# Performance work log

Hardware: AMD Instinct MI355X
Metric: run time of the kernel (lower is better)

The kernel has to match this reference:

```python
import jax, jax.numpy as jnp
import numpy as np

H = 128; D = 16; L = 4
NP_ = 50000; NL_ = 10000; EPP = 500000; ELP = 100000; EPL = 100000


def _rbf(d):
    # GaussianSmearing(start=0, stop=8, num_gaussians=16)
    off = jnp.linspace(0.0, 8.0, D)
    coeff = -0.5 / ((8.0 / (D - 1)) ** 2)
    x = d[:, None] - off[None, :]
    return jnp.exp(coeff * x * x)


def _layer_norm(x, w, b, eps=1e-5):
    mu = jnp.mean(x, axis=-1, keepdims=True)
    var = jnp.var(x, axis=-1, keepdims=True)
    return (x - mu) * jax.lax.rsqrt(var + eps) * w + b


def _block(x_src, x_dst, src, dst, ea, Wf_, bf_, Ws_, bs_, bnw, bnb, lnw, lnb):
    # CGConv message: z = [x_i(dst), x_j(src), edge_attr]
    z = jnp.concatenate([x_dst[dst], x_src[src], ea], axis=-1)  # [E, 2H+D]
    m = jax.nn.sigmoid(z @ Wf_ + bf_) * jax.nn.softplus(z @ Ws_ + bs_)
    agg = jax.ops.segment_sum(m, dst, num_segments=x_dst.shape[0])
    # BatchNorm1d in eval mode with running_mean=0, running_var=1
    agg = agg * (bnw / jnp.sqrt(1.0 + 1e-5)) + bnb
    out = agg + x_dst            # CGConv internal residual
    out = _layer_norm(out, lnw, lnb)
    out = jax.nn.relu(out)
    return out + x_dst           # ResidualCGConvBlock residual (dropout=identity in eval)


def setup_inputs() -> dict:
    key = jax.random.key(0)
    ks = jax.random.split(key, 16)
    s = lambda n: 1.0 / np.sqrt(n)
    inp = {
        'x_protein': jax.random.normal(ks[0], (NP_, 6), jnp.float32),
        'x_ligand': jax.random.normal(ks[1], (NL_, 6), jnp.float32),
        'ei_pp': jnp.stack([jax.random.randint(ks[2], (EPP,), 0, NP_),
                            jax.random.randint(ks[3], (EPP,), 0, NP_)]).astype(jnp.int32),
        'ea_pp': jax.random.uniform(ks[4], (EPP,), jnp.float32, 0.0, 8.0),
        'ei_lp': jnp.stack([jax.random.randint(ks[5], (ELP,), 0, NL_),
                            jax.random.randint(ks[6], (ELP,), 0, NP_)]).astype(jnp.int32),
        'ea_lp': jax.random.uniform(ks[7], (ELP,), jnp.float32, 0.0, 8.0),
        'ei_pl': jnp.stack([jax.random.randint(ks[8], (EPL,), 0, NP_),
                            jax.random.randint(ks[9], (EPL,), 0, NL_)]).astype(jnp.int32),
        'ea_pl': jax.random.uniform(ks[10], (EPL,), jnp.float32, 0.0, 8.0),
        'Wp': jax.random.normal(ks[11], (6, H), jnp.float32) * s(6),
        'bp': jnp.zeros((H,), jnp.float32),
        'Wl': jax.random.normal(ks[12], (6, H), jnp.float32) * s(6),
        'bl': jnp.zeros((H,), jnp.float32),
        'Wf': jax.random.normal(ks[13], (L, 3, 2 * H + D, H), jnp.float32) * s(2 * H + D),
        'bf': jnp.zeros((L, 3, H), jnp.float32),
        'Ws': jax.random.normal(ks[14], (L, 3, 2 * H + D, H), jnp.float32) * s(2 * H + D),
        'bs': jnp.zeros((L, 3, H), jnp.float32),
        'bn_w': jnp.ones((L, 3, H), jnp.float32),
        'bn_b': jnp.zeros((L, 3, H), jnp.float32),
        'ln_w': jnp.ones((L, 3, H), jnp.float32),
        'ln_b': jnp.zeros((L, 3, H), jnp.float32),
        'lno_w': jnp.ones((H,), jnp.float32),
        'lno_b': jnp.zeros((H,), jnp.float32),
        'fc_w': jax.random.normal(ks[15], (H, 21), jnp.float32) * s(H),
        'fc_b': jnp.zeros((21,), jnp.float32),
    }
    return inp


def reference(x_protein, x_ligand, ei_pp, ea_pp, ei_lp, ea_lp, ei_pl, ea_pl,
              Wp, bp, Wl, bl, Wf, bf, Ws, bs, bn_w, bn_b, ln_w, ln_b,
              lno_w, lno_b, fc_w, fc_b):
    xp = x_protein @ Wp + bp
    xl = x_ligand @ Wl + bl
    rpp = _rbf(ea_pp); rlp = _rbf(ea_lp); rpl = _rbf(ea_pl)
    for l in range(L):
        # HeteroConv aggr='sum': protein receives from pp and lp; ligand from pl
        p_pp = _block(xp, xp, ei_pp[0], ei_pp[1], rpp, Wf[l, 0], bf[l, 0], Ws[l, 0], bs[l, 0],
                      bn_w[l, 0], bn_b[l, 0], ln_w[l, 0], ln_b[l, 0])
        p_lp = _block(xl, xp, ei_lp[0], ei_lp[1], rlp, Wf[l, 1], bf[l, 1], Ws[l, 1], bs[l, 1],
                      bn_w[l, 1], bn_b[l, 1], ln_w[l, 1], ln_b[l, 1])
        l_pl = _block(xp, xl, ei_pl[0], ei_pl[1], rpl, Wf[l, 2], bf[l, 2], Ws[l, 2], bs[l, 2],
                      bn_w[l, 2], bn_b[l, 2], ln_w[l, 2], ln_b[l, 2])
        xp, xl = p_pp + p_lp, l_pl
    out = _layer_norm(xp, lno_w, lno_b)
    return out @ fc_w + fc_b
```

## Files before the change

### kernel.cpp

```cpp
#include <hip/hip_runtime.h>
#include <hip/hip_bf16.h>
#include <math.h>

#define H 128
#define LOG2E 1.44269504f

typedef __bf16 bf16x8 __attribute__((ext_vector_type(8)));
typedef float f32x4 __attribute__((ext_vector_type(4)));
typedef float f32x2 __attribute__((ext_vector_type(2)));
typedef __hip_bfloat16 bf16;
typedef unsigned int uint32;

static __device__ __forceinline__ float bf2f(bf16 v){ return __bfloat162float(v); }
static __device__ __forceinline__ bf16 f2bf(float v){ return __float2bfloat16(v); }
static __device__ __forceinline__ float u2f_lo(uint32 v){ return __uint_as_float(v << 16); }
static __device__ __forceinline__ float u2f_hi(uint32 v){ return __uint_as_float(v & 0xffff0000u); }

union bfpack { struct { bf16 lo, hi; } h; uint32 u; };
static __device__ __forceinline__ uint32 pack_bf2(float a, float b){
  bfpack p; p.h.lo = f2bf(a); p.h.hi = f2bf(b); return p.u;
}

static __device__ __forceinline__ int unperm64(int r){
  int base = r & ~63; int g = r & 63; int t = g >> 4; int j = g & 15;
  return base + 4*j + t;
}

#define NBIN 256
#define PREP_WP_N (4*1024*128)
#define PREP_WL_N (4*512*128)
#define RBF_N     (12*(NBIN+1)*128)

__global__ void prep_all(const float* __restrict__ Wf, const float* __restrict__ Ws,
                         const float* __restrict__ bfv, const float* __restrict__ bsv,
                         bf16* __restrict__ Wt_p, float* __restrict__ Bias_p,
                         bf16* __restrict__ Wt_l, float* __restrict__ Bias_l,
                         bf16* __restrict__ T2,
                         const float* __restrict__ Xp, const float* __restrict__ Wp,
                         const float* __restrict__ bp, float* __restrict__ Xpo,
                         bf16* __restrict__ Xpb, int NP,
                         const float* __restrict__ Xl, const float* __restrict__ Wl,
                         const float* __restrict__ bl, float* __restrict__ Xlo,
                         bf16* __restrict__ Xlb, int NL){
  int t = blockIdx.x*blockDim.x + threadIdx.x;
  if (t < PREP_WP_N){
    int k = t & 127; int idx = t >> 7;
    int rs = idx & 1023; int l = idx >> 10;
    int r = unperm64(rs);
    int rel, c, row0; const float* W; float bias = 0.f;
    if (r < 256)      { rel=0; c=r>>1;        row0=128; W = (r&1)?Ws:Wf; }
    else if (r < 512) { rel=2; c=(r-256)>>1;  row0=128; W = (r&1)?Ws:Wf; }
    else if (r < 640) { rel=0; c=r-512; row0=0; W=Wf; bias = bfv[(l*3+rel)*H+c]; }
    else if (r < 768) { rel=0; c=r-640; row0=0; W=Ws; bias = bsv[(l*3+rel)*H+c]; }
    else if (r < 896) { rel=1; c=r-768; row0=0; W=Wf; bias = bfv[(l*3+rel)*H+c]; }
    else              { rel=1; c=r-896; row0=0; W=Ws; bias = bsv[(l*3+rel)*H+c]; }
    Wt_p[t] = f2bf(LOG2E * W[((size_t)(l*3+rel)*272 + row0 + k)*H + c]);
    if (k == 0) Bias_p[l*1024 + r] = LOG2E * bias;
    return;
  }
  t -= PREP_WP_N;
  if (t < PREP_WL_N){
    int k = t & 127; int idx = t >> 7;
    int rs = idx & 511; int l = idx >> 9;
    int r = unperm64(rs);
    int rel, c, row0; const float* W; float bias = 0.f;
    if (r < 256)      { rel=1; c=r>>1;   row0=128; W = (r&1)?Ws:Wf; }
    else if (r < 384) { rel=2; c=r-256; row0=0; W=Wf; bias = bfv[(l*3+rel)*H+c]; }
    else              { rel=2; c=r-384; row0=0; W=Ws; bias = bsv[(l*3+rel)*H+c]; }
    Wt_l[t] = f2bf(LOG2E * W[((size_t)(l*3+rel)*272 + row0 + k)*H + c]);
    if (k == 0) Bias_l[l*512 + r] = LOG2E * bias;
    return;
  }
  t -= PREP_WL_N;
  if (t < RBF_N){
    int c = t & 127;
    int b = (t >> 7) % (NBIN+1);
    int pr = t / ((NBIN+1)*128);
    float d0 = (float)b * (8.0f/(float)NBIN);
    const float* wf = Wf + ((size_t)pr*272 + 256)*H + c;
    const float* ws = Ws + ((size_t)pr*272 + 256)*H + c;
    float f0=0.f, s0=0.f;
    #pragma unroll
    for (int k=0;k<16;k++){
      float o = 0.533333333f*(float)k;
      float tt = d0 - o;
      float r0 = __expf(-1.7578125f*tt*tt);
      f0 += r0*wf[(size_t)k*H]; s0 += r0*ws[(size_t)k*H];
    }
    bf16* o = T2 + ((size_t)(pr*(NBIN+1) + b))*256 + 2*c;
    o[0]=f2bf(LOG2E * f0); o[1]=f2bf(LOG2E * s0);
    return;
  }
  t -= RBF_N;
  {
    int idx = t;
    const float* Xin; const float* W; const float* b; float* Xout; bf16* Xbf;
    if (idx < NP*H){ Xin=Xp; W=Wp; b=bp; Xout=Xpo; Xbf=Xpb; }
    else { idx -= NP*H; if (idx >= NL*H) return; Xin=Xl; W=Wl; b=bl; Xout=Xlo; Xbf=Xlb; }
    int n = idx >> 7, c = idx & 127;
    float acc = b[c];
    #pragma unroll
    for (int k=0;k<6;k++) acc += Xin[n*6+k] * W[k*H+c];
    Xout[idx] = acc;
    Xbf[idx] = f2bf(acc);
  }
}

__global__ void hist3_k(const int* __restrict__ dpp, int Epp,
                        const int* __restrict__ dlp, int Elp,
                        const int* __restrict__ dpl, int Epl,
                        int* __restrict__ cpp, int* __restrict__ clp, int* __restrict__ cpl){
  int e = blockIdx.x*blockDim.x + threadIdx.x;
  if (e < Epp) atomicAdd(&cpp[dpp[e]], 1);
  else if (e < Epp+Elp) atomicAdd(&clp[dlp[e-Epp]], 1);
  else if (e < Epp+Elp+Epl) atomicAdd(&cpl[dpl[e-Epp-Elp]], 1);
}

#define SCH 1024

__global__ void __launch_bounds__(256) chunksum_k(
    const int* __restrict__ counts, int NP, int NL, int Cpp, int Cpl,
    int* __restrict__ chsum){
  __shared__ int wred[4];
  int b = blockIdx.x;
  const int* cnt; int n; int ch;
  if (b < Cpp){ cnt = counts; n = NP; ch = b; }
  else if (b < 2*Cpp){ cnt = counts + NP; n = NP; ch = b - Cpp; }
  else { cnt = counts + 2*NP; n = NL; ch = b - 2*Cpp; }
  int base = ch * SCH;
  int tid = threadIdx.x;
  int s = 0;
  #pragma unroll
  for (int j=0;j<SCH/256;j++){
    int i = base + tid + j*256;
    if (i < n) s += cnt[i];
  }
  #pragma unroll
  for (int o=32;o>=1;o>>=1) s += __shfl_xor(s,o,64);
  if ((tid & 63) == 0) wred[tid>>6] = s;
  __syncthreads();
  if (tid == 0) chsum[b] = wred[0]+wred[1]+wred[2]+wred[3];
}

__global__ void __launch_bounds__(192) scanmid_k(
    int* __restrict__ chsum, int Cpp, int Cpl, int NP, int NL,
    int* __restrict__ rp_pp, int* __restrict__ rp_lp, int* __restrict__ rp_pl){
  int wid = threadIdx.x >> 6, lane = threadIdx.x & 63;
  int C, off; int* rp_end; int n;
  if (wid == 0){ C = Cpp; off = 0;      rp_end = rp_pp; n = NP; }
  else if (wid == 1){ C = Cpp; off = Cpp; rp_end = rp_lp; n = NP; }
  else { C = Cpl; off = 2*Cpp; rp_end = rp_pl; n = NL; }
  int v = (lane < C) ? chsum[off + lane] : 0;
  int x = v;
  #pragma unroll
  for (int o=1;o<64;o<<=1){
    int y = __shfl_up(x, o, 64);
    if (lane >= o) x += y;
  }
  if (lane < C) chsum[off + lane] = x - v;
  if (lane == 63) rp_end[n] = x;
}

__global__ void __launch_bounds__(1024) scanfin_k(
    const int* __restrict__ counts, int NP, int NL, int Cpp, int Cpl,
    const int* __restrict__ chsum,
    int* __restrict__ rp_pp, int* __restrict__ cur_pp,
    int* __restrict__ rp_lp, int* __restrict__ cur_lp,
    int* __restrict__ rp_pl, int* __restrict__ cur_pl){
  __shared__ int wsum[16];
  int b = blockIdx.x;
  const int* cnt; int n, ch; int* rp; int* cur;
  if (b < Cpp){ cnt = counts; n = NP; ch = b; rp = rp_pp; cur = cur_pp; }
  else if (b < 2*Cpp){ cnt = counts + NP; n = NP; ch = b - Cpp; rp = rp_lp; cur = cur_lp; }
  else { cnt = counts + 2*NP; n = NL; ch = b - 2*Cpp; rp = rp_pl; cur = cur_pl; }
  int tid = threadIdx.x, lane = tid & 63, wid = tid >> 6;
  int i = ch*SCH + tid;
  int v = (i < n) ? cnt[i] : 0;
  int x = v;
  #pragma unroll
  for (int o=1;o<64;o<<=1){
    int y = __shfl_up(x, o, 64);
    if (lane >= o) x += y;
  }
  if (lane == 63) wsum[wid] = x;
  __syncthreads();
  if (wid == 0 && lane < 16){
    int w = wsum[lane];
    #pragma unroll
    for (int o=1;o<16;o<<=1){
      int y = __shfl_up(w, o, 64);
      if (lane >= o) w += y;
    }
    wsum[lane] = w;
  }
  __syncthreads();
  int waveoff = (wid == 0) ? 0 : wsum[wid-1];
  int ex = chsum[b] + waveoff + x - v;
  if (i < n){ rp[i] = ex; cur[i] = ex; }
}

__global__ void fill3_k(const int* __restrict__ ei_pp, const float* __restrict__ ea_pp, int Epp,
                        const int* __restrict__ ei_lp, const float* __restrict__ ea_lp, int Elp,
                        const int* __restrict__ ei_pl, const float* __restrict__ ea_pl, int Epl,
                        int* __restrict__ cur_pp, int2* __restrict__ e2_pp,
                        int* __restrict__ cur_lp, int2* __restrict__ e2_lp,
                        int* __restrict__ cur_pl, int2* __restrict__ e2_pl){
  int e = blockIdx.x*blockDim.x + threadIdx.x;
  if (e < Epp){
    int p = atomicAdd(&cur_pp[ei_pp[Epp + e]], 1);
    e2_pp[p] = make_int2(ei_pp[e], __float_as_int(ea_pp[e]));
  } else if (e < Epp+Elp){
    int i = e - Epp;
    int p = atomicAdd(&cur_lp[ei_lp[Elp + i]], 1);
    e2_lp[p] = make_int2(ei_lp[i], __float_as_int(ea_lp[i]));
  } else if (e < Epp+Elp+Epl){
    int i = e - Epp - Elp;
    int p = atomicAdd(&cur_pl[ei_pl[Epl + i]], 1);
    e2_pl[p] = make_int2(ei_pl[i], __float_as_int(ea_pl[i]));
  }
}

#define GR 8
__global__ void __launch_bounds__(256) gemm_tables(
    const bf16* __restrict__ Xp, const bf16* __restrict__ Wtp,
    const float* __restrict__ Biasp, bf16* __restrict__ Outp,
    int strips_p, int tasks_p,
    const bf16* __restrict__ Xl, const bf16* __restrict__ Wtl,
    const float* __restrict__ Biasl, bf16* __restrict__ Outl,
    int strips_l, int tasks_total){
  int wt = blockIdx.x*4 + (threadIdx.x >> 6);
  if (wt >= tasks_total) return;
  const bf16 *X, *Wt; const float* Bias; bf16* Out; int N, strips, g, chunk;
  if (wt < tasks_p){
    X=Xp; Wt=Wtp; Bias=Biasp; Out=Outp; N=1024; strips=strips_p;
    g = wt & 15; chunk = wt >> 4;
  } else {
    int w = wt - tasks_p;
    X=Xl; Wt=Wtl; Bias=Biasl; Out=Outl; N=512; strips=strips_l;
    g = w & 7; chunk = w >> 3;
  }
  int n0 = g << 6;
  int lane = threadIdx.x & 63;
  int lr = lane & 15, lq = lane >> 4;
  const bf16x8* B0 = (const bf16x8*)(const void*)(Wt + (size_t)(n0      + lr)*H);
  const bf16x8* B1 = (const bf16x8*)(const void*)(Wt + (size_t)(n0 + 16 + lr)*H);
  const bf16x8* B2 = (const bf16x8*)(const void*)(Wt + (size_t)(n0 + 32 + lr)*H);
  const bf16x8* B3 = (const bf16x8*)(const void*)(Wt + (size_t)(n0 + 48 + lr)*H);
  bf16x8 b0_0=B0[lq], b0_1=B0[4+lq], b0_2=B0[8+lq], b0_3=B0[12+lq];
  bf16x8 b1_0=B1[lq], b1_1=B1[4+lq], b1_2=B1[8+lq], b1_3=B1[12+lq];
  bf16x8 b2_0=B2[lq], b2_1=B2[4+lq], b2_2=B2[8+lq], b2_3=B2[12+lq];
  bf16x8 b3_0=B3[lq], b3_1=B3[4+lq], b3_2=B3[8+lq], b3_3=B3[12+lq];
  float4 bias = ((const float4*)(const void*)(Bias + n0))[lr];
  #pragma unroll 2
  for (int r=0;r<GR;r++){
    int strip = chunk*GR + r;
    if (strip >= strips) break;
    int m0 = strip << 4;
    const bf16x8* A = (const bf16x8*)(const void*)(X + (size_t)(m0+lr)*H);
    bf16x8 a0 = A[lq], a1 = A[4+lq], a2 = A[8+lq], a3 = A[12+lq];
    f32x4 acc0 = {0.f,0.f,0.f,0.f}, acc1 = acc0, acc2 = acc0, acc3 = acc0;
    acc0 = __builtin_amdgcn_mfma_f32_16x16x32_bf16(a0, b0_0, acc0, 0, 0, 0);
    acc1 = __builtin_amdgcn_mfma_f32_16x16x32_bf16(a0, b1_0, acc1, 0, 0, 0);
    acc2 = __builtin_amdgcn_mfma_f32_16x16x32_bf16(a0, b2_0, acc2, 0, 0, 0);
    acc3 = __builtin_amdgcn_mfma_f32_16x16x32_bf16(a0, b3_0, acc3, 0, 0, 0);
    acc0 = __builtin_amdgcn_mfma_f32_16x16x32_bf16(a1, b0_1, acc0, 0, 0, 0);
    acc1 = __builtin_amdgcn_mfma_f32_16x16x32_bf16(a1, b1_1, acc1, 0, 0, 0);
    acc2 = __builtin_amdgcn_mfma_f32_16x16x32_bf16(a1, b2_1, acc2, 0, 0, 0);
    acc3 = __builtin_amdgcn_mfma_f32_16x16x32_bf16(a1, b3_1, acc3, 0, 0, 0);
    acc0 = __builtin_amdgcn_mfma_f32_16x16x32_bf16(a2, b0_2, acc0, 0, 0, 0);
    acc1 = __builtin_amdgcn_mfma_f32_16x16x32_bf16(a2, b1_2, acc1, 0, 0, 0);
    acc2 = __builtin_amdgcn_mfma_f32_16x16x32_bf16(a2, b2_2, acc2, 0, 0, 0);
    acc3 = __builtin_amdgcn_mfma_f32_16x16x32_bf16(a2, b3_2, acc3, 0, 0, 0);
    acc0 = __builtin_amdgcn_mfma_f32_16x16x32_bf16(a3, b0_3, acc0, 0, 0, 0);
    acc1 = __builtin_amdgcn_mfma_f32_16x16x32_bf16(a3, b1_3, acc1, 0, 0, 0);
    acc2 = __builtin_amdgcn_mfma_f32_16x16x32_bf16(a3, b2_3, acc2, 0, 0, 0);
    acc3 = __builtin_amdgcn_mfma_f32_16x16x32_bf16(a3, b3_3, acc3, 0, 0, 0);
    #pragma unroll
    for (int rr=0;rr<4;rr++){
      int row = m0 + lq*4 + rr;
      uint2 pk;
      pk.x = pack_bf2(acc0[rr] + bias.x, acc1[rr] + bias.y);
      pk.y = pack_bf2(acc2[rr] + bias.z, acc3[rr] + bias.w);
      *(uint2*)(void*)(Out + (size_t)row*N + n0 + 4*lr) = pk;
    }
  }
}

static __device__ __forceinline__ float act_msg(float F, float S){
  float sig = __builtin_amdgcn_rcpf(1.f + __builtin_amdgcn_exp2f(-F));
  float e   = __builtin_amdgcn_exp2f(fminf(S, 86.f));
  float sp  = 0.69314718f * __builtin_amdgcn_logf(1.f + e);
  return sig * sp;
}

#define BN_RSQ 0.9999950000374997f

static __device__ __forceinline__ void edge_nb(uint2 g, uint2 t,
                                               f32x2 fd2, f32x2 sd2, f32x2& acc){
  f32x2 f2, s2;
  f2.x = u2f_lo(g.x) + u2f_lo(t.x);
  f2.y = u2f_lo(g.y) + u2f_lo(t.y);
  s2.x = u2f_hi(g.x) + u2f_hi(t.x);
  s2.y = u2f_hi(g.y) + u2f_hi(t.y);
  f2 += fd2; s2 += sd2;
  acc.x += act_msg(f2.x, s2.x);
  acc.y += act_msg(f2.y, s2.y);
}

static __device__ __forceinline__ void ln_stats_w(float v0, float v1, float& mu, float& var){
  float s = v0 + v1, q = v0*v0 + v1*v1;
  #pragma unroll
  for (int o=32;o>=1;o>>=1){ s += __shfl_xor(s,o,64); q += __shfl_xor(q,o,64); }
  mu = s * (1.f/128.f);
  var = q * (1.f/128.f) - mu*mu;
}

static __device__ __forceinline__ void aggregate(
    const int2* __restrict__ ev_arr, int e0, int e1,
    const uint2* __restrict__ G, int gstride, int goff,
    const uint2* __restrict__ Tb, int lane,
    f32x2 fd2, f32x2 sd2, f32x2& acc)
{
  for (int base = e0; base < e1; base += 64){
    int idx = base + lane;
    int2 ev = ev_arr[(idx < e1) ? idx : (e1-1)];
    float dd = __int_as_float(ev.y);
    int bnv = (int)__fmaf_rn(dd, (float)NBIN/8.0f, 0.5f);
    bnv = (bnv > NBIN) ? NBIN : bnv;
    int cnt = e1 - base; cnt = (cnt > 64) ? 64 : cnt;
    uint2 gA, tA, gB, tB, gC, tC;
    #define LDJ(gX, tX, j) { \
      int s_ = __builtin_amdgcn_readlane(ev.x, (j)); \
      int b_ = __builtin_amdgcn_readlane(bnv, (j)); \
      gX = G[(size_t)s_*gstride + goff + lane]; \
      tX = Tb[(size_t)b_*64 + lane]; }
    LDJ(gA, tA, 0);
    if (cnt > 1) LDJ(gB, tB, 1);
    if (cnt > 2) LDJ(gC, tC, 2);
    int j = 0;
    for (; j+5 < cnt; j += 3){
      edge_nb(gA, tA, fd2, sd2, acc); LDJ(gA, tA, j+3);
      edge_nb(gB, tB, fd2, sd2, acc); LDJ(gB, tB, j+4);
      edge_nb(gC, tC, fd2, sd2, acc); LDJ(gC, tC, j+5);
    }
    int rem = cnt - j;
    edge_nb(gA, tA, fd2, sd2, acc);
    if (rem > 3) LDJ(gA, tA, j+3);
    if (rem > 1) edge_nb(gB, tB, fd2, sd2, acc);
    if (rem > 4) LDJ(gB, tB, j+4);
    if (rem > 2) edge_nb(gC, tC, fd2, sd2, acc);
    if (rem > 3) edge_nb(gA, tA, fd2, sd2, acc);
    if (rem > 4) edge_nb(gB, tB, fd2, sd2, acc);
    #undef LDJ
  }
}

__global__ void __launch_bounds__(256) node_update(
    const bf16* __restrict__ PT, const bf16* __restrict__ LT,
    const float* __restrict__ xp, const float* __restrict__ xl,
    const int* __restrict__ pp_rp, const int2* __restrict__ pp_e2,
    const int* __restrict__ lp_rp, const int2* __restrict__ lp_e2,
    const int* __restrict__ pl_rp, const int2* __restrict__ pl_e2,
    const bf16* __restrict__ T2,
    const float* __restrict__ bn_w, const float* __restrict__ bn_b,
    const float* __restrict__ ln_w, const float* __restrict__ ln_b,
    float* __restrict__ xp_out, bf16* __restrict__ xp_bf,
    float* __restrict__ xl_out, bf16* __restrict__ xl_bf,
    int layer, int NP, int NL, int PB)
{
  int wave = threadIdx.x >> 6;
  int lane = threadIdx.x & 63;
  const uint2* PTg = (const uint2*)(const void*)PT;
  if ((int)blockIdx.x < PB){
    int node = blockIdx.x*4 + wave;
    if (node >= NP) return;
    float2 x = ((const float2*)(const void*)(xp + (size_t)node*H))[lane];
    const uint32* PTu = (const uint32*)(const void*)PT;
    const uint2*  LTg = (const uint2*)(const void*)LT;
    float o1_0, o1_1, o2_0, o2_1;
    {
      int pr = layer*3 + 0;
      uint32 fdp = PTu[(size_t)node*512 + 256 + lane];
      uint32 sdp = PTu[(size_t)node*512 + 320 + lane];
      const uint2* Tb = (const uint2*)(const void*)(T2 + (size_t)pr*(NBIN+1)*256);
      f32x2 fd2 = {u2f_lo(fdp), u2f_hi(fdp)};
      f32x2 sd2 = {u2f_lo(sdp), u2f_hi(sdp)};
      f32x2 acc = {0.f, 0.f};
      aggregate(pp_e2, pp_rp[node], pp_rp[node+1], PTg, 256, 0, Tb, lane, fd2, sd2, acc);
      float2 bw = ((const float2*)(const void*)(bn_w + pr*H))[lane];
      float2 bb = ((const float2*)(const void*)(bn_b + pr*H))[lane];
      float2 lw = ((const float2*)(const void*)(ln_w + pr*H))[lane];
      float2 lb = ((const float2*)(const void*)(ln_b + pr*H))[lane];
      float v0 = acc.x * (bw.x * BN_RSQ) + bb.x + x.x;
      float v1 = acc.y * (bw.y * BN_RSQ) + bb.y + x.y;
      float mu, var; ln_stats_w(v0, v1, mu, var);
      float rs = rsqrtf(var + 1e-5f);
      o1_0 = fmaxf((v0-mu)*rs*lw.x + lb.x, 0.f) + x.x;
      o1_1 = fmaxf((v1-mu)*rs*lw.y + lb.y, 0.f) + x.y;
    }
    {
      int pr = layer*3 + 1;
      uint32 fdp = PTu[(size_t)node*512 + 384 + lane];
      uint32 sdp = PTu[(size_t)node*512 + 448 + lane];
      const uint2* Tb = (const uint2*)(const void*)(T2 + (size_t)pr*(NBIN+1)*256);
      f32x2 fd2 = {u2f_lo(fdp), u2f_hi(fdp)};
      f32x2 sd2 = {u2f_lo(sdp), u2f_hi(sdp)};
      f32x2 acc = {0.f, 0.f};
      aggregate(lp_e2, lp_rp[node], lp_rp[node+1], LTg, 128, 0, Tb, lane, fd2, sd2, acc);
      float2 bw = ((const float2*)(const void*)(bn_w + pr*H))[lane];
      float2 bb = ((const float2*)(const void*)(bn_b + pr*H))[lane];
      float2 lw = ((const float2*)(const void*)(ln_w + pr*H))[lane];
      float2 lb = ((const float2*)(const void*)(ln_b + pr*H))[lane];
      float v0 = acc.x * (bw.x * BN_RSQ) + bb.x + x.x;
      float v1 = acc.y * (bw.y * BN_RSQ) + bb.y + x.y;
      float mu, var; ln_stats_w(v0, v1, mu, var);
      float rs = rsqrtf(var + 1e-5f);
      o2_0 = fmaxf((v0-mu)*rs*lw.x + lb.x, 0.f) + x.x;
      o2_1 = fmaxf((v1-mu)*rs*lw.y + lb.y, 0.f) + x.y;
    }
    float out0 = o1_0 + o2_0, out1 = o1_1 + o2_1;
    ((float2*)(void*)(xp_out + (size_t)node*H))[lane] = make_float2(out0, out1);
    ((uint32*)(void*)(xp_bf + (size_t)node*H))[lane] = pack_bf2(out0, out1);
  } else {
    int node = (blockIdx.x - PB)*4 + wave;
    if (node >= NL) return;
    float2 x = ((const float2*)(const void*)(xl + (size_t)node*H))[lane];
    const uint32* LTu = (const uint32*)(const void*)LT;
    int pr = layer*3 + 2;
    uint32 fdp = LTu[(size_t)node*256 + 128 + lane];
    uint32 sdp = LTu[(size_t)node*256 + 192 + lane];
    const uint2* Tb = (const uint2*)(const void*)(T2 + (size_t)pr*(NBIN+1)*256);
    f32x2 fd2 = {u2f_lo(fdp), u2f_hi(fdp)};
    f32x2 sd2 = {u2f_lo(sdp), u2f_hi(sdp)};
    f32x2 acc = {0.f, 0.f};
    aggregate(pl_e2, pl_rp[node], pl_rp[node+1], PTg, 256, 64, Tb, lane, fd2, sd2, acc);
    float2 bw = ((const float2*)(const void*)(bn_w + pr*H))[lane];
    float2 bb = ((const float2*)(const void*)(bn_b + pr*H))[lane];
    float2 lw = ((const float2*)(const void*)(ln_w + pr*H))[lane];
    float2 lb = ((const float2*)(const void*)(ln_b + pr*H))[lane];
    float v0 = acc.x * (bw.x * BN_RSQ) + bb.x + x.x;
    float v1 = acc.y * (bw.y * BN_RSQ) + bb.y + x.y;
    float mu, var; ln_stats_w(v0, v1, mu, var);
    float rs = rsqrtf(var + 1e-5f);
    float out0 = fmaxf((v0-mu)*rs*lw.x + lb.x, 0.f) + x.x;
    float out1 = fmaxf((v1-mu)*rs*lw.y + lb.y, 0.f) + x.y;
    ((float2*)(void*)(xl_out + (size_t)node*H))[lane] = make_float2(out0, out1);
    ((uint32*)(void*)(xl_bf + (size_t)node*H))[lane] = pack_bf2(out0, out1);
  }
}

__global__ void __launch_bounds__(128) final_k(const float* __restrict__ xp,
    const float* __restrict__ lnw, const float* __restrict__ lnb,
    const float* __restrict__ fcw, const float* __restrict__ fcb,
    float* __restrict__ out, int N){
  __shared__ float sm[4];
  __shared__ float lnv[128];
  int node = blockIdx.x, c = threadIdx.x;
  float v = xp[(size_t)node*H + c];
  float s = v, q = v*v;
  #pragma unroll
  for (int o=32;o>=1;o>>=1){ s += __shfl_xor(s,o,64); q += __shfl_xor(q,o,64); }
  __syncthreads();
  if ((c & 63) == 0){ sm[(c>>6)*2] = s; sm[(c>>6)*2+1] = q; }
  __syncthreads();
  float S = sm[0] + sm[2], Q = sm[1] + sm[3];
  float mu = S * (1.f/128.f);
  float var = Q * (1.f/128.f) - mu*mu;
  float ln = (v-mu)*rsqrtf(var+1e-5f)*lnw[c] + lnb[c];
  lnv[c] = ln;
  __syncthreads();
  if (c < 21){
    float a = fcb[c];
    #pragma unroll 4
    for (int i=0;i<128;i++) a += lnv[i]*fcw[i*21+c];
    out[(size_t)node*21 + c] = a;
  }
}

extern "C" void kernel_launch(void* const* d_in, const int* in_sizes, int n_in,
                              void* d_out, int out_size, void* d_ws, size_t ws_size,
                              hipStream_t stream){
  const float* x_protein = (const float*)d_in[0];
  const float* x_ligand  = (const float*)d_in[1];
  const int*   ei_pp = (const int*)d_in[2];
  const float* ea_pp = (const float*)d_in[3];
  const int*   ei_lp = (const int*)d_in[4];
  const float* ea_lp = (const float*)d_in[5];
  const int*   ei_pl = (const int*)d_in[6];
  const float* ea_pl = (const float*)d_in[7];
  const float* Wp  = (const float*)d_in[8];
  const float* bp  = (const float*)d_in[9];
  const float* Wl  = (const float*)d_in[10];
  const float* bl  = (const float*)d_in[11];
  const float* Wf  = (const float*)d_in[12];
  const float* bfv = (const float*)d_in[13];
  const float* Wsv = (const float*)d_in[14];
  const float* bsv = (const float*)d_in[15];
  const float* bn_w = (const float*)d_in[16];
  const float* bn_b = (const float*)d_in[17];
  const float* ln_w = (const float*)d_in[18];
  const float* ln_b = (const float*)d_in[19];
  const float* lno_w = (const float*)d_in[20];
  const float* lno_b = (const float*)d_in[21];
  const float* fc_w = (const float*)d_in[22];
  const float* fc_b = (const float*)d_in[23];

  int NP  = in_sizes[0]/6, NL = in_sizes[1]/6;
  int EPP = in_sizes[3], ELP = in_sizes[5], EPL = in_sizes[7];

  char* ws = (char*)d_ws;
  size_t off = 0;
  auto alloc = [&](size_t bytes)->void*{
    void* p = ws + off; off = (off + bytes + 255) & ~(size_t)255; return p;
  };

  float* xpA = (float*)alloc((size_t)NP*H*4);
  float* xpB = (float*)alloc((size_t)NP*H*4);
  float* xlA = (float*)alloc((size_t)NL*H*4);
  float* xlB = (float*)alloc((size_t)NL*H*4);
  bf16* xp_bf = (bf16*)alloc((size_t)NP*H*2);
  bf16* xl_bf = (bf16*)alloc((size_t)NL*H*2);
  bf16* PT    = (bf16*)alloc((size_t)NP*1024*2);
  bf16* LT    = (bf16*)alloc((size_t)NL*512*2);
  bf16* Wt_p  = (bf16*)alloc((size_t)4*1024*H*2);
  bf16* Wt_l  = (bf16*)alloc((size_t)4*512*H*2);
  float* Bias_p = (float*)alloc((size_t)4*1024*4);
  float* Bias_l = (float*)alloc((size_t)4*512*4);
  bf16* T2    = (bf16*)alloc((size_t)12*(NBIN+1)*256*2);
  int* counts = (int*)alloc((size_t)(2*NP+NL)*4);
  int* rp_pp  = (int*)alloc((size_t)(NP+1)*4);
  int* cur_pp = (int*)alloc((size_t)NP*4);
  int* rp_lp  = (int*)alloc((size_t)(NP+1)*4);
  int* cur_lp = (int*)alloc((size_t)NP*4);
  int* rp_pl  = (int*)alloc((size_t)(NL+1)*4);
  int* cur_pl = (int*)alloc((size_t)NL*4);
  int2* e2_pp = (int2*)alloc((size_t)EPP*8);
  int2* e2_lp = (int2*)alloc((size_t)ELP*8);
  int2* e2_pl = (int2*)alloc((size_t)EPL*8);
  int Cpp = (NP + SCH - 1) / SCH;
  int Cpl = (NL + SCH - 1) / SCH;
  int* chsum = (int*)alloc((size_t)(2*Cpp + Cpl)*4);
  (void)ws_size; (void)n_in; (void)out_size;

  size_t prep_total = (size_t)PREP_WP_N + PREP_WL_N + RBF_N + (size_t)(NP+NL)*H;
  prep_all<<<(prep_total+255)/256, 256, 0, stream>>>(Wf, Wsv, bfv, bsv,
      Wt_p, Bias_p, Wt_l, Bias_l, T2,
      x_protein, Wp, bp, xpA, xp_bf, NP,
      x_ligand,  Wl, bl, xlA, xl_bf, NL);
  hipMemsetAsync(counts, 0, (size_t)(2*NP+NL)*4, stream);
  int* cnt_pp = counts; int* cnt_lp = counts + NP; int* cnt_pl = counts + 2*NP;
  int Etot = EPP + ELP + EPL;
  hist3_k<<<(Etot+255)/256, 256, 0, stream>>>(ei_pp+EPP, EPP, ei_lp+ELP, ELP, ei_pl+EPL, EPL,
                                              cnt_pp, cnt_lp, cnt_pl);
  chunksum_k<<<2*Cpp + Cpl, 256, 0, stream>>>(counts, NP, NL, Cpp, Cpl, chsum);
  scanmid_k<<<1, 192, 0, stream>>>(chsum, Cpp, Cpl, NP, NL, rp_pp, rp_lp, rp_pl);
  scanfin_k<<<2*Cpp + Cpl, 1024, 0, stream>>>(counts, NP, NL, Cpp, Cpl, chsum,
                                              rp_pp, cur_pp, rp_lp, cur_lp, rp_pl, cur_pl);
  fill3_k<<<(Etot+255)/256, 256, 0, stream>>>(ei_pp, ea_pp, EPP, ei_lp, ea_lp, ELP,
                                              ei_pl, ea_pl, EPL,
                                              cur_pp, e2_pp, cur_lp, e2_lp, cur_pl, e2_pl);

  float* xp_cur = xpA; float* xp_nxt = xpB;
  float* xl_cur = xlA; float* xl_nxt = xlB;
  int strips_p = NP >> 4, strips_l = NL >> 4;
  int tasks_p = 16 * ((strips_p + GR - 1) / GR);
  int tasks_l = 8  * ((strips_l + GR - 1) / GR);
  int tasks_total = tasks_p + tasks_l;
  int PB = (NP + 3) / 4, LB = (NL + 3) / 4;
  for (int l=0; l<4; l++){
    gemm_tables<<<(tasks_total+3)/4, 256, 0, stream>>>(
        xp_bf, Wt_p + (size_t)l*1024*H, Bias_p + l*1024, PT, strips_p, tasks_p,
        xl_bf, Wt_l + (size_t)l*512*H,  Bias_l + l*512,  LT, strips_l, tasks_total);
    node_update<<<PB + LB, 256, 0, stream>>>(PT, LT, xp_cur, xl_cur,
        rp_pp, e2_pp, rp_lp, e2_lp, rp_pl, e2_pl, T2,
        bn_w, bn_b, ln_w, ln_b, xp_nxt, xp_bf, xl_nxt, xl_bf, l, NP, NL, PB);
    float* t;
    t = xp_cur; xp_cur = xp_nxt; xp_nxt = t;
    t = xl_cur; xl_cur = xl_nxt; xl_nxt = t;
  }

  final_k<<<NP, 128, 0, stream>>>(xp_cur, lno_w, lno_b, fc_w, fc_b, (float*)d_out, NP);
}
```

Measured before the change: 817.5 us.

## Process nodes in descending-degree order via degree-binned permutation in node_update

Adds three setup kernels that bucket protein and ligand nodes by in-degree (capped at 63), scan the buckets and scatter a permutation that lists high-degree nodes first. node_update then maps each wave to perm[idx] instead of the node with the same index. Handling heavy nodes first and grouping nodes of similar degree into the same block is meant to reduce tail imbalance and intra-block divergence. The cost is an extra indirection per wave, less locality for the xp/PT rows, and three small launches added to setup.

```diff
diff --git a/kernel.cpp b/kernel.cpp
--- a/kernel.cpp
+++ b/kernel.cpp
@@ -217,6 +217,72 @@
     int i = e - Epp - Elp;
     int p = atomicAdd(&cur_pl[ei_pl[Epl + i]], 1);
     e2_pl[p] = make_int2(ei_pl[i], __float_as_int(ea_pl[i]));
+  }
+}
+
+__global__ void __launch_bounds__(256) degbin_hist(
+    const int* __restrict__ rp_pp, const int* __restrict__ rp_lp,
+    const int* __restrict__ rp_pl, int NP, int NL, int* __restrict__ hist){
+  __shared__ int lh[128];
+  int t = threadIdx.x;
+  if (t < 128) lh[t] = 0;
+  __syncthreads();
+  int i = blockIdx.x*256 + t;
+  if (i < NP){
+    int d = (rp_pp[i+1]-rp_pp[i]) + (rp_lp[i+1]-rp_lp[i]);
+    if (d > 63) d = 63;
+    atomicAdd(&lh[63 - d], 1);
+  } else if (i < NP+NL){
+    int n = i - NP;
+    int d = rp_pl[n+1]-rp_pl[n];
+    if (d > 63) d = 63;
+    atomicAdd(&lh[64 + 63 - d], 1);
+  }
+  __syncthreads();
+  if (t < 128 && lh[t]) atomicAdd(&hist[t], lh[t]);
+}
+
+__global__ void __launch_bounds__(128) degbin_scan(
+    const int* __restrict__ hist, int* __restrict__ cursor){
+  int t = threadIdx.x, lane = t & 63;
+  int v = hist[t];
+  int x = v;
+  #pragma unroll
+  for (int o=1;o<64;o<<=1){
+    int y = __shfl_up(x, o, 64);
+    if (lane >= o) x += y;
+  }
+  cursor[t] = x - v;
+}
+
+__global__ void __launch_bounds__(256) degbin_scatter(
+    const int* __restrict__ rp_pp, const int* __restrict__ rp_lp,
+    const int* __restrict__ rp_pl, int NP, int NL,
+    int* __restrict__ cursor, int* __restrict__ perm){
+  __shared__ int lh[128], lbase[128], lrank[128];
+  int t = threadIdx.x;
+  if (t < 128){ lh[t] = 0; lrank[t] = 0; }
+  __syncthreads();
+  int i = blockIdx.x*256 + t;
+  int bin = -1, n = 0;
+  if (i < NP){
+    n = i;
+    int d = (rp_pp[i+1]-rp_pp[i]) + (rp_lp[i+1]-rp_lp[i]);
+    if (d > 63) d = 63;
+    bin = 63 - d;
+  } else if (i < NP+NL){
+    n = i - NP;
+    int d = rp_pl[n+1]-rp_pl[n];
+    if (d > 63) d = 63;
+    bin = 64 + 63 - d;
+  }
+  if (bin >= 0) atomicAdd(&lh[bin], 1);
+  __syncthreads();
+  if (t < 128 && lh[t]) lbase[t] = atomicAdd(&cursor[t], lh[t]);
+  __syncthreads();
+  if (bin >= 0){
+    int r = atomicAdd(&lrank[bin], 1);
+    perm[(bin < 64 ? 0 : NP) + lbase[bin] + r] = n;
   }
 }
 
@@ -364,6 +430,7 @@
     const bf16* __restrict__ T2,
     const float* __restrict__ bn_w, const float* __restrict__ bn_b,
     const float* __restrict__ ln_w, const float* __restrict__ ln_b,
+    const int* __restrict__ perm,
     float* __restrict__ xp_out, bf16* __restrict__ xp_bf,
     float* __restrict__ xl_out, bf16* __restrict__ xl_bf,
     int layer, int NP, int NL, int PB)
@@ -372,8 +439,9 @@
   int lane = threadIdx.x & 63;
   const uint2* PTg = (const uint2*)(const void*)PT;
   if ((int)blockIdx.x < PB){
-    int node = blockIdx.x*4 + wave;
-    if (node >= NP) return;
+    int idx = blockIdx.x*4 + wave;
+    if (idx >= NP) return;
+    int node = perm[idx];
     float2 x = ((const float2*)(const void*)(xp + (size_t)node*H))[lane];
     const uint32* PTu = (const uint32*)(const void*)PT;
     const uint2*  LTg = (const uint2*)(const void*)LT;
@@ -422,8 +490,9 @@
     ((float2*)(void*)(xp_out + (size_t)node*H))[lane] = make_float2(out0, out1);
     ((uint32*)(void*)(xp_bf + (size_t)node*H))[lane] = pack_bf2(out0, out1);
   } else {
-    int node = (blockIdx.x - PB)*4 + wave;
-    if (node >= NL) return;
+    int idx = (blockIdx.x - PB)*4 + wave;
+    if (idx >= NL) return;
+    int node = perm[NP + idx];
     float2 x = ((const float2*)(const void*)(xl + (size_t)node*H))[lane];
     const uint32* LTu = (const uint32*)(const void*)LT;
     int pr = layer*3 + 2;
@@ -540,6 +609,9 @@
   int Cpp = (NP + SCH - 1) / SCH;
   int Cpl = (NL + SCH - 1) / SCH;
   int* chsum = (int*)alloc((size_t)(2*Cpp + Cpl)*4);
+  int* dhist  = (int*)alloc(128*4);
+  int* dcur   = (int*)alloc(128*4);
+  int* perm   = (int*)alloc((size_t)(NP+NL)*4);
   (void)ws_size; (void)n_in; (void)out_size;
 
   size_t prep_total = (size_t)PREP_WP_N + PREP_WL_N + RBF_N + (size_t)(NP+NL)*H;
@@ -548,6 +620,7 @@
       x_protein, Wp, bp, xpA, xp_bf, NP,
       x_ligand,  Wl, bl, xlA, xl_bf, NL);
   hipMemsetAsync(counts, 0, (size_t)(2*NP+NL)*4, stream);
+  hipMemsetAsync(dhist, 0, 128*4, stream);
   int* cnt_pp = counts; int* cnt_lp = counts + NP; int* cnt_pl = counts + 2*NP;
   int Etot = EPP + ELP + EPL;
   hist3_k<<<(Etot+255)/256, 256, 0, stream>>>(ei_pp+EPP, EPP, ei_lp+ELP, ELP, ei_pl+EPL, EPL,
@@ -559,6 +632,10 @@
   fill3_k<<<(Etot+255)/256, 256, 0, stream>>>(ei_pp, ea_pp, EPP, ei_lp, ea_lp, ELP,
                                               ei_pl, ea_pl, EPL,
                                               cur_pp, e2_pp, cur_lp, e2_lp, cur_pl, e2_pl);
+  int nbks = (NP + NL + 255) / 256;
+  degbin_hist<<<nbks, 256, 0, stream>>>(rp_pp, rp_lp, rp_pl, NP, NL, dhist);
+  degbin_scan<<<1, 128, 0, stream>>>(dhist, dcur);
+  degbin_scatter<<<nbks, 256, 0, stream>>>(rp_pp, rp_lp, rp_pl, NP, NL, dcur, perm);
 
   float* xp_cur = xpA; float* xp_nxt = xpB;
   float* xl_cur = xlA; float* xl_nxt = xlB;
@@ -573,7 +650,7 @@
         xl_bf, Wt_l + (size_t)l*512*H,  Bias_l + l*512,  LT, strips_l, tasks_total);
     node_update<<<PB + LB, 256, 0, stream>>>(PT, LT, xp_cur, xl_cur,
         rp_pp, e2_pp, rp_lp, e2_lp, rp_pl, e2_pl, T2,
-        bn_w, bn_b, ln_w, ln_b, xp_nxt, xp_bf, xl_nxt, xl_bf, l, NP, NL, PB);
+        bn_w, bn_b, ln_w, ln_b, perm, xp_nxt, xp_bf, xl_nxt, xl_bf, l, NP, NL, PB);
     float* t;
     t = xp_cur; xp_cur = xp_nxt; xp_nxt = t;
     t = xl_cur; xl_cur = xl_nxt; xl_nxt = t;
```

Result: no change. 822.5 us (+0.6%).
